# Kernel optimization log

Hardware: AMD Instinct MI355X
Metric: run time of the kernel (lower is better)

## Reference

```python
import jax, jax.numpy as jnp
from jax import lax
import numpy as np

EPS = 1e-5
NEG_SLOPE = 0.1
POOL = 2


def _cond_block(x, w, b, fcw, fcb, g, be, rm, rv):
    """CondConv1d(k=3,pad=1,num_experts=e) + BatchNorm1d(eval) + LeakyReLU(0.1).
    x: (B, Cin, W); w: (E, Cout, Cin, 3); b: (E, Cout); fcw: (E, Cin); fcb: (E,)
    """
    # routing: adaptive avg pool to 1 -> fc -> sigmoid  => (B, E)
    r = jax.nn.sigmoid(x.mean(axis=-1) @ fcw.T + fcb)
    # per-sample mixed weights/bias
    cw = jnp.einsum('be,eoik->boik', r, w)          # (B, Cout, Cin, 3)
    cb = r @ b                                      # (B, Cout)
    # batched per-sample conv1d (same padding, stride 1)
    def one(xi, wi):
        return lax.conv_general_dilated(
            xi[None], wi, window_strides=(1,), padding=[(1, 1)],
            dimension_numbers=('NCH', 'OIH', 'NCH'))[0]
    y = jax.vmap(one)(x, cw) + cb[:, :, None]       # (B, Cout, W)
    # BatchNorm1d in eval mode (running stats)
    y = (y - rm[None, :, None]) * (g[None, :, None] / jnp.sqrt(rv[None, :, None] + EPS)) + be[None, :, None]
    # LeakyReLU(0.1)
    return jnp.where(y >= 0, y, NEG_SLOPE * y)


def setup_inputs() -> dict:
    key = jax.random.key(0)
    ks = jax.random.split(key, 16)
    B, W = 32, 2048
    chans = [64, 128, 256]
    E = 1  # num_experts default
    inp = {'x': jax.random.normal(ks[0], (B, chans[0], W), dtype=jnp.float32)}
    i = 1
    for li, (ci, co) in enumerate(zip(chans[:-1], chans[1:]), start=1):
        fan_in = ci * 3
        wb = float(np.sqrt(6.0 / fan_in))  # kaiming_uniform a=sqrt(5) scale approx
        bb = float(1.0 / np.sqrt(fan_in))
        inp[f'w{li}'] = jax.random.uniform(ks[i], (E, co, ci, 3), minval=-wb, maxval=wb, dtype=jnp.float32); i += 1
        inp[f'b{li}'] = jax.random.uniform(ks[i], (E, co), minval=-bb, maxval=bb, dtype=jnp.float32); i += 1
        inp[f'fcw{li}'] = jax.random.normal(ks[i], (E, ci), dtype=jnp.float32) * 0.05; i += 1
        inp[f'fcb{li}'] = jnp.zeros((E,), dtype=jnp.float32)
        inp[f'g{li}'] = 1.0 + 0.1 * jax.random.normal(ks[i], (co,), dtype=jnp.float32); i += 1
        inp[f'be{li}'] = 0.1 * jax.random.normal(ks[i], (co,), dtype=jnp.float32); i += 1
        inp[f'rm{li}'] = 0.1 * jax.random.normal(ks[i], (co,), dtype=jnp.float32); i += 1
        inp[f'rv{li}'] = 0.5 + jax.random.uniform(ks[i], (co,), dtype=jnp.float32); i += 1
    return inp


def reference(x, w1, b1, fcw1, fcb1, g1, be1, rm1, rv1,
              w2, b2, fcw2, fcb2, g2, be2, rm2, rv2):
    y = _cond_block(x, w1, b1, fcw1, fcb1, g1, be1, rm1, rv1)
    y = _cond_block(y, w2, b2, fcw2, fcb2, g2, be2, rm2, rv2)
    # max_pool1d(kernel=stride=POOL)
    B, C, W = y.shape
    y = y.reshape(B, C, W // POOL, POOL).max(axis=-1)
    # dropout: eval mode -> identity
    return y
```

## Files before the change

kernel.cpp:

```cpp
#include <hip/hip_runtime.h>
#include <hip/hip_bf16.h>
#include <math.h>

#define BATCH 32
#define WLEN  2048

typedef __attribute__((ext_vector_type(8))) short short8;
typedef __attribute__((ext_vector_type(4))) short short4v;
typedef __attribute__((ext_vector_type(4))) float floatx4;

__device__ inline short f2bf(float f) {
  unsigned u = __float_as_uint(f);
  unsigned r = (u + 0x7fffu + ((u >> 16) & 1u)) >> 16;
  return (short)r;
}

__global__ __launch_bounds__(256) void fused_prep(
    const float* __restrict__ w1, const float* __restrict__ w2,
    const float* __restrict__ x, const float* __restrict__ fcw1,
    short* __restrict__ wp1, short* __restrict__ wp2,
    float* __restrict__ racc1) {
  const int blk = blockIdx.x;
  const int tid = threadIdx.x;
  if (blk < 12) {
    int iw = blk * 256 + tid;
    int o = iw & 127;
    int t = iw >> 7;
    int ig = t & 7;
    int k = t >> 3;
    short8 v;
#pragma unroll
    for (int e = 0; e < 8; ++e) v[e] = f2bf(w1[(o * 64 + ig * 8 + e) * 3 + k]);
    *(short8*)(wp1 + (size_t)iw * 8) = v;
  } else if (blk < 60) {
    int iw = (blk - 12) * 256 + tid;
    int o = iw & 255;
    int t = iw >> 8;
    int ig = t & 15;
    int k = t >> 4;
    short8 v;
#pragma unroll
    for (int e = 0; e < 8; ++e) v[e] = f2bf(w2[(o * 128 + ig * 8 + e) * 3 + k]);
    *(short8*)(wp2 + (size_t)iw * 8) = v;
  } else {
    int t = blk - 60;
    int j = t & 7, b = t >> 3;
    const float4* xb = (const float4*)(x + ((size_t)b * 64 + j * 8) * WLEN);
    float sum = 0.f;
    for (int idx = tid; idx < 8 * 512; idx += 256) {
      int c = idx >> 9;
      float4 v = xb[idx];
      sum += (v.x + v.y + v.z + v.w) * fcw1[j * 8 + c];
    }
    __shared__ float red[256];
    red[tid] = sum;
    __syncthreads();
    for (int s = 128; s > 0; s >>= 1) {
      if (tid < s) red[tid] += red[tid + s];
      __syncthreads();
    }
    if (tid == 0) racc1[b * 8 + j] = red[0];
  }
}

__global__ __launch_bounds__(256) void conv1_mfma(
    const float* __restrict__ x, const short* __restrict__ wp1,
    const float* __restrict__ bias, const float* __restrict__ g,
    const float* __restrict__ be, const float* __restrict__ rm,
    const float* __restrict__ rv, const float* __restrict__ racc1,
    const float* __restrict__ fcb, const float* __restrict__ fcw2,
    short* __restrict__ y1p, float* __restrict__ racc2) {
  const int b = blockIdx.y;
  const int wt = blockIdx.x;
  const int w0 = wt * 64;
  const int tid = threadIdx.x;
  const int wave = tid >> 6, lane = tid & 63;
  const int ln = lane & 15, kg = lane >> 4;
  const int oh = wave & 1, wq = wave >> 1;

  __shared__ short xs[8 * 66 * 8];
  __shared__ float red[256];

  const float* xb = x + (size_t)b * 64 * WLEN;
  for (int idx = tid; idx < 8 * 66; idx += 256) {
    int ig = idx / 66;
    int p = idx - ig * 66;
    int w = w0 - 1 + p;
    short8 v = {0, 0, 0, 0, 0, 0, 0, 0};
    if ((unsigned)w < (unsigned)WLEN) {
      const float* src = xb + (size_t)(ig * 8) * WLEN + w;
#pragma unroll
      for (int e = 0; e < 8; ++e) v[e] = f2bf(src[(size_t)e * WLEN]);
    }
    *(short8*)(xs + idx * 8) = v;
  }
  __syncthreads();

  floatx4 acc[4][2];
#pragma unroll
  for (int ms = 0; ms < 4; ++ms)
#pragma unroll
    for (int ns = 0; ns < 2; ++ns) acc[ms][ns] = (floatx4){0.f, 0.f, 0.f, 0.f};

#pragma unroll
  for (int q = 0; q < 2; ++q) {
#pragma unroll
    for (int k = 0; k < 3; ++k) {
      short8 af[4];
      const short* wk =
          wp1 + ((size_t)(k * 8 + q * 4 + kg) * 128 + oh * 64 + ln) * 8;
#pragma unroll
      for (int ms = 0; ms < 4; ++ms)
        af[ms] = *(const short8*)(wk + (size_t)ms * 16 * 8);
#pragma unroll
      for (int ns = 0; ns < 2; ++ns) {
        short8 bf = *(const short8*)(
            xs + ((q * 4 + kg) * 66 + wq * 32 + ns * 16 + ln + k) * 8);
#pragma unroll
        for (int ms = 0; ms < 4; ++ms)
          acc[ms][ns] = __builtin_amdgcn_mfma_f32_16x16x32_bf16(
              af[ms], bf, acc[ms][ns], 0, 0, 0);
      }
    }
  }

  float zs = 0.f;
#pragma unroll
  for (int qq = 0; qq < 8; ++qq) zs += racc1[b * 8 + qq];
  float z = zs * (1.f / (float)WLEN) + fcb[0];
  float r1v = 1.f / (1.f + expf(-z));

  float rsum2 = 0.f;
#pragma unroll
  for (int ms = 0; ms < 4; ++ms) {
    const int o0 = oh * 64 + ms * 16 + kg * 4;
    float a_[4], c_[4], fw[4];
#pragma unroll
    for (int rr = 0; rr < 4; ++rr) {
      int o = o0 + rr;
      float s = g[o] * rsqrtf(rv[o] + 1e-5f);
      a_[rr] = r1v * s;
      c_[rr] = (r1v * bias[o] - rm[o]) * s + be[o];
      fw[rr] = fcw2[o];
    }
#pragma unroll
    for (int ns = 0; ns < 2; ++ns) {
      int w = w0 + wq * 32 + ns * 16 + ln;
      short4v pk;
#pragma unroll
      for (int rr = 0; rr < 4; ++rr) {
        float v = acc[ms][ns][rr] * a_[rr] + c_[rr];
        v = v >= 0.f ? v : 0.1f * v;
        rsum2 += v * fw[rr];
        pk[rr] = f2bf(v);
      }
      *(short4v*)(y1p + ((size_t)(b * 16 + (o0 >> 3)) * WLEN + w) * 8 + (o0 & 7)) = pk;
    }
  }
  red[tid] = rsum2;
  __syncthreads();
  for (int s = 128; s > 0; s >>= 1) {
    if (tid < s) red[tid] += red[tid + s];
    __syncthreads();
  }
  if (tid == 0) racc2[b * 32 + wt] = red[0];
}

__global__ __launch_bounds__(512) void conv2_mfma(
    const short* __restrict__ y1p, const short* __restrict__ wp2,
    const float* __restrict__ bias, const float* __restrict__ g,
    const float* __restrict__ be, const float* __restrict__ rm,
    const float* __restrict__ rv, const float* __restrict__ racc2,
    const float* __restrict__ fcb, float* __restrict__ out) {
  const int b = blockIdx.y;
  const int w0 = blockIdx.x * 64;
  const int tid = threadIdx.x;
  const int wave = tid >> 6, lane = tid & 63;
  const int ln = lane & 15, kg = lane >> 4;
  const int oq = wave & 3, wh = wave >> 2;

  __shared__ short xs[16 * 66 * 8];

  const short* yb = y1p + (size_t)b * 16 * WLEN * 8;
  for (int idx = tid; idx < 16 * 66; idx += 512) {
    int ig = idx / 66;
    int p = idx - ig * 66;
    int w = w0 - 1 + p;
    short8 v = {0, 0, 0, 0, 0, 0, 0, 0};
    if ((unsigned)w < (unsigned)WLEN)
      v = *(const short8*)(yb + ((size_t)ig * WLEN + w) * 8);
    *(short8*)(xs + idx * 8) = v;
  }
  __syncthreads();

  floatx4 acc[4][2];
#pragma unroll
  for (int ms = 0; ms < 4; ++ms)
#pragma unroll
    for (int ns = 0; ns < 2; ++ns) acc[ms][ns] = (floatx4){0.f, 0.f, 0.f, 0.f};

#pragma unroll
  for (int q = 0; q < 4; ++q) {
#pragma unroll
    for (int k = 0; k < 3; ++k) {
      short8 af[4];
      const short* wk =
          wp2 + ((size_t)(k * 16 + q * 4 + kg) * 256 + oq * 64 + ln) * 8;
#pragma unroll
      for (int ms = 0; ms < 4; ++ms)
        af[ms] = *(const short8*)(wk + (size_t)ms * 16 * 8);
#pragma unroll
      for (int ns = 0; ns < 2; ++ns) {
        short8 bf = *(const short8*)(
            xs + ((q * 4 + kg) * 66 + wh * 32 + ns * 16 + ln + k) * 8);
#pragma unroll
        for (int ms = 0; ms < 4; ++ms)
          acc[ms][ns] = __builtin_amdgcn_mfma_f32_16x16x32_bf16(
              af[ms], bf, acc[ms][ns], 0, 0, 0);
      }
    }
  }

  float zs = 0.f;
#pragma unroll
  for (int t = 0; t < 32; ++t) zs += racc2[b * 32 + t];
  float z = zs * (1.f / (float)WLEN) + fcb[0];
  float r2v = 1.f / (1.f + expf(-z));

#pragma unroll
  for (int ms = 0; ms < 4; ++ms) {
    const int o0 = oq * 64 + ms * 16 + kg * 4;
    float a_[4], c_[4];
#pragma unroll
    for (int rr = 0; rr < 4; ++rr) {
      int o = o0 + rr;
      float s = g[o] * rsqrtf(rv[o] + 1e-5f);
      a_[rr] = r2v * s;
      c_[rr] = (r2v * bias[o] - rm[o]) * s + be[o];
    }
    float m0[4], m1[4];
#pragma unroll
    for (int half = 0; half < 2; ++half) {
#pragma unroll
      for (int rr = 0; rr < 4; ++rr) {
        float v = acc[ms][half][rr] * a_[rr] + c_[rr];
        v = v >= 0.f ? v : 0.1f * v;
        float m = fmaxf(v, __shfl_xor(v, 1));
        if (half == 0) m0[rr] = m; else m1[rr] = m;
      }
    }
    const int pc = (w0 >> 1) + wh * 16 + ln;
#pragma unroll
    for (int rr = 0; rr < 4; ++rr) {
      int src = kg * 16 + ((ln & 7) << 1);
      float aa = __shfl(m0[rr], src);
      float bb = __shfl(m1[rr], src);
      float val = (ln < 8) ? aa : bb;
      out[((size_t)(b * 256 + o0 + rr)) * (WLEN / 2) + pc] = val;
    }
  }
}

extern "C" void kernel_launch(void* const* d_in, const int* in_sizes, int n_in,
                              void* d_out, int out_size, void* d_ws, size_t ws_size,
                              hipStream_t stream) {
  const float* x    = (const float*)d_in[0];
  const float* w1   = (const float*)d_in[1];
  const float* b1   = (const float*)d_in[2];
  const float* fcw1 = (const float*)d_in[3];
  const float* fcb1 = (const float*)d_in[4];
  const float* g1   = (const float*)d_in[5];
  const float* be1  = (const float*)d_in[6];
  const float* rm1  = (const float*)d_in[7];
  const float* rv1  = (const float*)d_in[8];
  const float* w2   = (const float*)d_in[9];
  const float* b2   = (const float*)d_in[10];
  const float* fcw2 = (const float*)d_in[11];
  const float* fcb2 = (const float*)d_in[12];
  const float* g2   = (const float*)d_in[13];
  const float* be2  = (const float*)d_in[14];
  const float* rm2  = (const float*)d_in[15];
  const float* rv2  = (const float*)d_in[16];
  float* out = (float*)d_out;

  char* ws = (char*)d_ws;
  short* y1p   = (short*)ws;
  short* wp1   = (short*)(ws + (size_t)16 * 1024 * 1024);
  short* wp2   = (short*)(ws + (size_t)16 * 1024 * 1024 + 65536);
  float* racc1 = (float*)(ws + (size_t)16 * 1024 * 1024 + 327680);
  float* racc2 = racc1 + 256;

  fused_prep<<<316, 256, 0, stream>>>(w1, w2, x, fcw1, wp1, wp2, racc1);
  conv1_mfma<<<dim3(32, 32), 256, 0, stream>>>(
      x, wp1, b1, g1, be1, rm1, rv1, racc1, fcb1, fcw2, y1p, racc2);
  conv2_mfma<<<dim3(32, 32), 512, 0, stream>>>(
      y1p, wp2, b2, g2, be2, rm2, rv2, racc2, fcb2, out);
}
```

Baseline: 55.94 us.

## Double width tiles, stage conv weights in LDS with double-buffered prefetch

Both conv kernels now cover 128 output positions per block instead of 64, which halves the grid and the halo overhead. conv1 copies the whole packed weight tensor into shared memory once per block and uses 512 threads. conv2 streams weight chunks through a double-buffered LDS buffer, prefetching the next chunk into registers while the MFMAs run, with a 4x4 accumulator tile per wave. The aim is to cut repeated global and L2 weight reads and improve operand reuse. In exchange it uses more LDS and registers, adds a barrier per chunk, and leaves fewer blocks to fill the machine.

```diff
diff --git a/kernel.cpp b/kernel.cpp
--- a/kernel.cpp
+++ b/kernel.cpp
@@ -63,7 +63,7 @@
   }
 }
 
-__global__ __launch_bounds__(256) void conv1_mfma(
+__global__ __launch_bounds__(512, 4) void conv1_mfma(
     const float* __restrict__ x, const short* __restrict__ wp1,
     const float* __restrict__ bias, const float* __restrict__ g,
     const float* __restrict__ be, const float* __restrict__ rm,
@@ -71,20 +71,23 @@
     const float* __restrict__ fcb, const float* __restrict__ fcw2,
     short* __restrict__ y1p, float* __restrict__ racc2) {
   const int b = blockIdx.y;
-  const int wt = blockIdx.x;
-  const int w0 = wt * 64;
+  const int w0 = blockIdx.x * 128;
   const int tid = threadIdx.x;
   const int wave = tid >> 6, lane = tid & 63;
   const int ln = lane & 15, kg = lane >> 4;
   const int oh = wave & 1, wq = wave >> 1;
 
-  __shared__ short xs[8 * 66 * 8];
-  __shared__ float red[256];
+  __shared__ short wl[3 * 8 * 128 * 8];
+  __shared__ short xs[8 * 130 * 8];
+  __shared__ float red[512];
+
+  for (int i = tid; i < 3072; i += 512)
+    *(short8*)(wl + (size_t)i * 8) = *(const short8*)(wp1 + (size_t)i * 8);
 
   const float* xb = x + (size_t)b * 64 * WLEN;
-  for (int idx = tid; idx < 8 * 66; idx += 256) {
-    int ig = idx / 66;
-    int p = idx - ig * 66;
+  for (int idx = tid; idx < 8 * 130; idx += 512) {
+    int ig = idx / 130;
+    int p = idx - ig * 130;
     int w = w0 - 1 + p;
     short8 v = {0, 0, 0, 0, 0, 0, 0, 0};
     if ((unsigned)w < (unsigned)WLEN) {
@@ -106,21 +109,21 @@
   for (int q = 0; q < 2; ++q) {
 #pragma unroll
     for (int k = 0; k < 3; ++k) {
-      short8 af[4];
-      const short* wk =
-          wp1 + ((size_t)(k * 8 + q * 4 + kg) * 128 + oh * 64 + ln) * 8;
+      short8 af[4], bf[2];
+      const short* wk = wl + ((size_t)(k * 8 + q * 4 + kg) * 128 + oh * 64 + ln) * 8;
 #pragma unroll
       for (int ms = 0; ms < 4; ++ms)
         af[ms] = *(const short8*)(wk + (size_t)ms * 16 * 8);
 #pragma unroll
-      for (int ns = 0; ns < 2; ++ns) {
-        short8 bf = *(const short8*)(
-            xs + ((q * 4 + kg) * 66 + wq * 32 + ns * 16 + ln + k) * 8);
-#pragma unroll
-        for (int ms = 0; ms < 4; ++ms)
+      for (int ns = 0; ns < 2; ++ns)
+        bf[ns] = *(const short8*)(
+            xs + ((q * 4 + kg) * 130 + wq * 32 + ns * 16 + ln + k) * 8);
+#pragma unroll
+      for (int ms = 0; ms < 4; ++ms)
+#pragma unroll
+        for (int ns = 0; ns < 2; ++ns)
           acc[ms][ns] = __builtin_amdgcn_mfma_f32_16x16x32_bf16(
-              af[ms], bf, acc[ms][ns], 0, 0, 0);
-      }
+              af[ms], bf[ns], acc[ms][ns], 0, 0, 0);
     }
   }
 
@@ -159,71 +162,94 @@
   }
   red[tid] = rsum2;
   __syncthreads();
-  for (int s = 128; s > 0; s >>= 1) {
+  for (int s = 256; s > 0; s >>= 1) {
     if (tid < s) red[tid] += red[tid + s];
     __syncthreads();
   }
-  if (tid == 0) racc2[b * 32 + wt] = red[0];
-}
-
-__global__ __launch_bounds__(512) void conv2_mfma(
+  if (tid == 0) racc2[b * 16 + blockIdx.x] = red[0];
+}
+
+__global__ __launch_bounds__(512, 4) void conv2_mfma(
     const short* __restrict__ y1p, const short* __restrict__ wp2,
     const float* __restrict__ bias, const float* __restrict__ g,
     const float* __restrict__ be, const float* __restrict__ rm,
     const float* __restrict__ rv, const float* __restrict__ racc2,
     const float* __restrict__ fcb, float* __restrict__ out) {
   const int b = blockIdx.y;
-  const int w0 = blockIdx.x * 64;
+  const int w0 = blockIdx.x * 128;
   const int tid = threadIdx.x;
   const int wave = tid >> 6, lane = tid & 63;
   const int ln = lane & 15, kg = lane >> 4;
   const int oq = wave & 3, wh = wave >> 2;
 
-  __shared__ short xs[16 * 66 * 8];
+  __shared__ short xs[16 * 130 * 8];
+  __shared__ short wbuf[2][8192];
 
   const short* yb = y1p + (size_t)b * 16 * WLEN * 8;
-  for (int idx = tid; idx < 16 * 66; idx += 512) {
-    int ig = idx / 66;
-    int p = idx - ig * 66;
+  for (int idx = tid; idx < 16 * 130; idx += 512) {
+    int ig = idx / 130;
+    int p = idx - ig * 130;
     int w = w0 - 1 + p;
     short8 v = {0, 0, 0, 0, 0, 0, 0, 0};
     if ((unsigned)w < (unsigned)WLEN)
       v = *(const short8*)(yb + ((size_t)ig * WLEN + w) * 8);
     *(short8*)(xs + idx * 8) = v;
   }
+
+  {
+    const short* src = wp2;
+    *(short8*)(wbuf[0] + (size_t)(0 * 512 + tid) * 8) =
+        *(const short8*)(src + (size_t)(0 * 512 + tid) * 8);
+    *(short8*)(wbuf[0] + (size_t)(1 * 512 + tid) * 8) =
+        *(const short8*)(src + (size_t)(1 * 512 + tid) * 8);
+  }
   __syncthreads();
 
-  floatx4 acc[4][2];
+  floatx4 acc[4][4];
 #pragma unroll
   for (int ms = 0; ms < 4; ++ms)
 #pragma unroll
-    for (int ns = 0; ns < 2; ++ns) acc[ms][ns] = (floatx4){0.f, 0.f, 0.f, 0.f};
-
-#pragma unroll
-  for (int q = 0; q < 4; ++q) {
-#pragma unroll
-    for (int k = 0; k < 3; ++k) {
-      short8 af[4];
-      const short* wk =
-          wp2 + ((size_t)(k * 16 + q * 4 + kg) * 256 + oq * 64 + ln) * 8;
-#pragma unroll
-      for (int ms = 0; ms < 4; ++ms)
-        af[ms] = *(const short8*)(wk + (size_t)ms * 16 * 8);
-#pragma unroll
-      for (int ns = 0; ns < 2; ++ns) {
-        short8 bf = *(const short8*)(
-            xs + ((q * 4 + kg) * 66 + wh * 32 + ns * 16 + ln + k) * 8);
-#pragma unroll
-        for (int ms = 0; ms < 4; ++ms)
-          acc[ms][ns] = __builtin_amdgcn_mfma_f32_16x16x32_bf16(
-              af[ms], bf, acc[ms][ns], 0, 0, 0);
-      }
-    }
+    for (int ns = 0; ns < 4; ++ns) acc[ms][ns] = (floatx4){0.f, 0.f, 0.f, 0.f};
+
+#pragma unroll
+  for (int c = 0; c < 12; ++c) {
+    const int cur = c & 1;
+    const int q = c / 3, k = c % 3;
+
+    short8 nreg0, nreg1;
+    if (c < 11) {
+      const int nq = (c + 1) / 3, nk = (c + 1) % 3;
+      const short* src = wp2 + (size_t)(nk * 16 + nq * 4) * 256 * 8;
+      nreg0 = *(const short8*)(src + (size_t)(0 * 512 + tid) * 8);
+      nreg1 = *(const short8*)(src + (size_t)(1 * 512 + tid) * 8);
+    }
+
+    short8 af[4], bf[4];
+#pragma unroll
+    for (int ms = 0; ms < 4; ++ms)
+      af[ms] = *(const short8*)(
+          wbuf[cur] + (size_t)(kg * 256 + oq * 64 + ms * 16 + ln) * 8);
+#pragma unroll
+    for (int ns = 0; ns < 4; ++ns)
+      bf[ns] = *(const short8*)(
+          xs + ((q * 4 + kg) * 130 + wh * 64 + ns * 16 + ln + k) * 8);
+#pragma unroll
+    for (int ms = 0; ms < 4; ++ms)
+#pragma unroll
+      for (int ns = 0; ns < 4; ++ns)
+        acc[ms][ns] = __builtin_amdgcn_mfma_f32_16x16x32_bf16(
+            af[ms], bf[ns], acc[ms][ns], 0, 0, 0);
+
+    if (c < 11) {
+      *(short8*)(wbuf[cur ^ 1] + (size_t)(0 * 512 + tid) * 8) = nreg0;
+      *(short8*)(wbuf[cur ^ 1] + (size_t)(1 * 512 + tid) * 8) = nreg1;
+    }
+    __syncthreads();
   }
 
   float zs = 0.f;
 #pragma unroll
-  for (int t = 0; t < 32; ++t) zs += racc2[b * 32 + t];
+  for (int t = 0; t < 16; ++t) zs += racc2[b * 16 + t];
   float z = zs * (1.f / (float)WLEN) + fcb[0];
   float r2v = 1.f / (1.f + expf(-z));
 
@@ -238,25 +264,29 @@
       a_[rr] = r2v * s;
       c_[rr] = (r2v * bias[o] - rm[o]) * s + be[o];
     }
-    float m0[4], m1[4];
-#pragma unroll
-    for (int half = 0; half < 2; ++half) {
+#pragma unroll
+    for (int np = 0; np < 2; ++np) {
+      float m0[4], m1[4];
+#pragma unroll
+      for (int half = 0; half < 2; ++half) {
+        int ns = np * 2 + half;
+#pragma unroll
+        for (int rr = 0; rr < 4; ++rr) {
+          float v = acc[ms][ns][rr] * a_[rr] + c_[rr];
+          v = v >= 0.f ? v : 0.1f * v;
+          float m = fmaxf(v, __shfl_xor(v, 1));
+          if (half == 0) m0[rr] = m; else m1[rr] = m;
+        }
+      }
+      const int pc = (w0 >> 1) + wh * 32 + np * 16 + ln;
 #pragma unroll
       for (int rr = 0; rr < 4; ++rr) {
-        float v = acc[ms][half][rr] * a_[rr] + c_[rr];
-        v = v >= 0.f ? v : 0.1f * v;
-        float m = fmaxf(v, __shfl_xor(v, 1));
-        if (half == 0) m0[rr] = m; else m1[rr] = m;
+        int src = kg * 16 + ((ln & 7) << 1);
+        float aa = __shfl(m0[rr], src);
+        float bb = __shfl(m1[rr], src);
+        float val = (ln < 8) ? aa : bb;
+        out[((size_t)(b * 256 + o0 + rr)) * (WLEN / 2) + pc] = val;
       }
-    }
-    const int pc = (w0 >> 1) + wh * 16 + ln;
-#pragma unroll
-    for (int rr = 0; rr < 4; ++rr) {
-      int src = kg * 16 + ((ln & 7) << 1);
-      float aa = __shfl(m0[rr], src);
-      float bb = __shfl(m1[rr], src);
-      float val = (ln < 8) ? aa : bb;
-      out[((size_t)(b * 256 + o0 + rr)) * (WLEN / 2) + pc] = val;
     }
   }
 }
@@ -291,8 +321,8 @@
   float* racc2 = racc1 + 256;
 
   fused_prep<<<316, 256, 0, stream>>>(w1, w2, x, fcw1, wp1, wp2, racc1);
-  conv1_mfma<<<dim3(32, 32), 256, 0, stream>>>(
+  conv1_mfma<<<dim3(16, 32), 512, 0, stream>>>(
       x, wp1, b1, g1, be1, rm1, rv1, racc1, fcb1, fcw2, y1p, racc2);
-  conv2_mfma<<<dim3(32, 32), 512, 0, stream>>>(
+  conv2_mfma<<<dim3(16, 32), 512, 0, stream>>>(
       y1p, wp2, b2, g2, be2, rm2, rv2, racc2, fcb2, out);
 }
```

After: 54.50 us. 1.03x faster.
